# Kernel tuning notes

Hardware: AMD Instinct MI355X
Metric: run time of the kernel (lower is better)

## Reference

```python
import jax, jax.numpy as jnp
import numpy as np

B, S, D, H, L, FF, V, NB, G, C = 8, 1024, 256, 8, 2, 1024, 32000, 20000, 12, 4
DH = D // H


def _layer_norm(x, g, b, eps=1e-5):
    m = x.mean(-1, keepdims=True)
    v = ((x - m) ** 2).mean(-1, keepdims=True)
    return (x - m) / jnp.sqrt(v + eps) * g + b


def setup_inputs() -> dict:
    key = jax.random.key(0)
    ks = jax.random.split(key, 32)
    w = lambda k, shape, s=0.05: (jax.random.normal(k, shape, dtype=jnp.float32) * s)
    inp = {
        'input_ids': jax.random.randint(ks[0], (B, S), 0, V),
        'ngram_ids': jax.random.randint(ks[1], (V, G), 0, NB),
        'tfidf_scores': jax.random.uniform(ks[2], (V,), dtype=jnp.float32),
        'emb': jax.random.uniform(ks[3], (V, D), minval=-0.1, maxval=0.1, dtype=jnp.float32).at[0].set(0.0),  # padding_idx=0 row zeroed
        'pos_enc': jax.random.normal(ks[4], (1, S, D), dtype=jnp.float32) * 0.01,
        'bucket_emb': jax.random.uniform(ks[5], (NB, D), minval=-0.05, maxval=0.05, dtype=jnp.float32),
        'Wq': w(ks[6], (L, D, D)), 'bq': jnp.zeros((L, D)),
        'Wk': w(ks[7], (L, D, D)), 'bk': jnp.zeros((L, D)),
        'Wv': w(ks[8], (L, D, D)), 'bv': jnp.zeros((L, D)),
        'Wo': w(ks[9], (L, D, D)), 'bo': jnp.zeros((L, D)),
        'g1': jnp.ones((L, D)), 'be1': jnp.zeros((L, D)),
        'g2': jnp.ones((L, D)), 'be2': jnp.zeros((L, D)),
        'W1': w(ks[10], (L, D, FF)), 'b1': jnp.zeros((L, FF)),
        'W2': w(ks[11], (L, FF, D)), 'b2': jnp.zeros((L, D)),
        'alpha': jnp.full((L,), 0.1, dtype=jnp.float32),
        'gf': jnp.ones((D,)), 'bf': jnp.zeros((D,)),
        'Wc': jax.random.uniform(ks[12], (D, C), minval=-0.1, maxval=0.1, dtype=jnp.float32),
        'bc': jnp.zeros((C,)),
    }
    return inp


def reference(input_ids, ngram_ids, tfidf_scores, emb, pos_enc, bucket_emb,
              Wq, bq, Wk, bk, Wv, bv, Wo, bo, g1, be1, g2, be2,
              W1, b1, W2, b2, alpha, gf, bf, Wc, bc):
    pad_mask = input_ids == 0                      # (B,S) key padding mask
    x = emb[input_ids] + pos_enc[:, :S]            # (B,S,D)
    # char n-gram embedding: masked mean over n-gram buckets
    tok_ng = ngram_ids[jnp.clip(input_ids, 0, ngram_ids.shape[0] - 1)]   # (B,S,G)
    e_ng = bucket_emb[tok_ng]                       # (B,S,G,D)
    m = (tok_ng != 0)[..., None].astype(x.dtype)
    x = x + (e_ng * m).sum(axis=2) / jnp.clip(m.sum(axis=2), 1.0, None)
    # TF-IDF bias per key position
    bias_base = tfidf_scores[jnp.clip(input_ids, 0, tfidf_scores.shape[0] - 1)]  # (B,S)
    scale = DH ** -0.5
    for l in range(L):
        x2 = _layer_norm(x, g1[l], be1[l])
        Q = (x2 @ Wq[l] + bq[l]).reshape(B, S, H, DH).transpose(0, 2, 1, 3)
        K = (x2 @ Wk[l] + bk[l]).reshape(B, S, H, DH).transpose(0, 2, 1, 3)
        Vv = (x2 @ Wv[l] + bv[l]).reshape(B, S, H, DH).transpose(0, 2, 1, 3)
        scores = jnp.einsum('bhqd,bhkd->bhqk', Q, K) * scale
        scores = scores + (bias_base * alpha[l])[:, None, None, :]
        scores = jnp.where(pad_mask[:, None, None, :], -jnp.inf, scores)
        attn = jax.nn.softmax(scores, axis=-1)
        out = jnp.einsum('bhqk,bhkd->bhqd', attn, Vv).transpose(0, 2, 1, 3).reshape(B, S, D)
        x = x + (out @ Wo[l] + bo[l])
        x2 = _layer_norm(x, g2[l], be2[l])
        x = x + (jax.nn.relu(x2 @ W1[l] + b1[l]) @ W2[l] + b2[l])
    x = _layer_norm(x, gf, bf)
    return x[:, 0] @ Wc + bc                        # CLS pooling -> (B,4)
```

## Files before the change

### kernel.cpp

```cpp
#include <hip/hip_runtime.h>
#include <hip/hip_bf16.h>
#include <math.h>

#define TOK 8192
#define DIM 256
#define SEQ 1024
#define NH 8
#define FFD 1024
#define NL 2
#define VOCAB 32000
#define QKSTRIDE 2097152

typedef short bf16x8 __attribute__((ext_vector_type(8)));
typedef float f32x4 __attribute__((ext_vector_type(4)));

__device__ __forceinline__ ushort f2bf(float f) {
  union { float f; uint32_t u; } v; v.f = f;
  uint32_t r = v.u + 0x7FFFu + ((v.u >> 16) & 1u);
  return (ushort)(r >> 16);
}

__device__ __forceinline__ float bf2f(ushort u) {
  union { uint32_t u; float f; } v; v.u = (uint32_t)u << 16; return v.f;
}

__device__ __forceinline__ float exp2_n(float x) {
  float r; asm("v_exp_f32 %0, %1" : "=v"(r) : "v"(x)); return r;
}

__device__ __forceinline__ uint32_t cvtpk(float lo, float hi) {
  uint32_t r; asm("v_cvt_pk_bf16_f32 %0, %1, %2" : "=v"(r) : "v"(lo), "v"(hi));
  return r;
}

__device__ __forceinline__ void gload_lds16(const ushort* gp, ushort* lp) {
  __builtin_amdgcn_global_load_lds(
      (const __attribute__((address_space(1))) void*)gp,
      (__attribute__((address_space(3))) void*)lp, 16, 0, 0);
}

__global__ __launch_bounds__(256) void embed_ln_kernel(
    const int* __restrict__ ids, const int* __restrict__ ngram_ids,
    const float* __restrict__ tfidf, const float* __restrict__ emb,
    const float* __restrict__ pos, const float* __restrict__ bucket,
    const float* __restrict__ alpha, const float* __restrict__ g1,
    const float* __restrict__ be1,
    float* __restrict__ x, ushort* __restrict__ x2b, float* __restrict__ bm2)
{
  __shared__ int ngs[12];
  __shared__ float red[2][4];
  const int t = blockIdx.x;
  const int id = ids[t];
  int idc = id; if (idc < 0) idc = 0; if (idc > VOCAB-1) idc = VOCAB-1;
  if (threadIdx.x < 12) ngs[threadIdx.x] = ngram_ids[idc*12 + threadIdx.x];
  if (threadIdx.x == 0) {
    const float tf = tfidf[idc];
    const bool msk = (id == 0);
    const float l2e = 1.4426950408889634f;
    bm2[t]       = msk ? -1e30f : tf * alpha[0] * l2e;
    bm2[TOK + t] = msk ? -1e30f : tf * alpha[1] * l2e;
  }
  __syncthreads();
  const int d = threadIdx.x;
  const int s = t & (SEQ - 1);
  float v = emb[(size_t)id*DIM + d] + pos[s*DIM + d];
  float sum = 0.f; int cnt = 0;
  #pragma unroll
  for (int g = 0; g < 12; ++g) {
    const int ng = ngs[g];
    if (ng != 0) { sum += bucket[(size_t)ng*DIM + d]; cnt++; }
  }
  v += sum / fmaxf((float)cnt, 1.0f);
  x[(size_t)t*DIM + d] = v;
  const int wave = d >> 6, lane = d & 63;
  float sm = v;
  #pragma unroll
  for (int o = 32; o >= 1; o >>= 1) sm += __shfl_xor(sm, o);
  if (lane == 0) red[0][wave] = sm;
  __syncthreads();
  const float mean = (red[0][0]+red[0][1]+red[0][2]+red[0][3]) * (1.f/256.f);
  const float dv = v - mean;
  float q = dv * dv;
  #pragma unroll
  for (int o = 32; o >= 1; o >>= 1) q += __shfl_xor(q, o);
  if (lane == 0) red[1][wave] = q;
  __syncthreads();
  const float var = (red[1][0]+red[1][1]+red[1][2]+red[1][3]) * (1.f/256.f);
  const float rs = rsqrtf(var + 1e-5f);
  x2b[(size_t)t*DIM + d] = f2bf(dv*rs*g1[d] + be1[d]);
}

__global__ __launch_bounds__(256) void ln_bf16(
    const float* __restrict__ x, const float* __restrict__ g,
    const float* __restrict__ b, ushort* __restrict__ y)
{
  const int wave = threadIdx.x >> 6, lane = threadIdx.x & 63;
  const int row = blockIdx.x * 4 + wave;
  const float* xr = x + (size_t)row * DIM;
  float4 v = *reinterpret_cast<const float4*>(xr + lane*4);
  float s = v.x + v.y + v.z + v.w;
  #pragma unroll
  for (int o = 32; o >= 1; o >>= 1) s += __shfl_xor(s, o);
  const float mean = s * (1.f/256.f);
  const float dx0 = v.x-mean, dx1 = v.y-mean, dx2 = v.z-mean, dx3 = v.w-mean;
  float q = dx0*dx0 + dx1*dx1 + dx2*dx2 + dx3*dx3;
  #pragma unroll
  for (int o = 32; o >= 1; o >>= 1) q += __shfl_xor(q, o);
  const float rs = rsqrtf(q * (1.f/256.f) + 1e-5f);
  float4 gv = *reinterpret_cast<const float4*>(g + lane*4);
  float4 bv = *reinterpret_cast<const float4*>(b + lane*4);
  ushort4 o4;
  o4.x = f2bf(dx0*rs*gv.x + bv.x);
  o4.y = f2bf(dx1*rs*gv.y + bv.y);
  o4.z = f2bf(dx2*rs*gv.z + bv.z);
  o4.w = f2bf(dx3*rs*gv.w + bv.w);
  *reinterpret_cast<ushort4*>(y + (size_t)row*DIM + lane*4) = o4;
}

struct TDesc { const float* src; ushort* dst; int K; int N; };
struct TDescs { TDesc d[12]; };

__global__ __launch_bounds__(256) void transpose_conv(TDescs descs)
{
  const TDesc t = descs.d[blockIdx.z];
  const int k0 = blockIdx.x * 32, n0 = blockIdx.y * 32;
  if (k0 >= t.K || n0 >= t.N) return;
  __shared__ float tile[32][33];
  const int r = threadIdx.x >> 5, cc = threadIdx.x & 31;
  #pragma unroll
  for (int i = 0; i < 4; ++i)
    tile[r + i*8][cc] = t.src[(size_t)(k0 + r + i*8)*t.N + n0 + cc];
  __syncthreads();
  #pragma unroll
  for (int i = 0; i < 4; ++i)
    t.dst[(size_t)(n0 + r + i*8)*t.K + k0 + cc] = f2bf(tile[cc][r + i*8]);
}

template<int KDIM, int NDIM, int MODE>
__global__ __launch_bounds__(256) void gemm_mfma(
    const ushort* __restrict__ A, const ushort* __restrict__ Bw,
    const float* __restrict__ bias0, const float* __restrict__ bias1,
    const float* __restrict__ bias2, void* __restrict__ Cout,
    ushort* __restrict__ vtb)
{
  __shared__ ushort Al[3][64*32];
  __shared__ ushort Bl[3][128*32];
  const int bm = blockIdx.y * 64, bn = blockIdx.x * 128;
  const int tid = threadIdx.x, w = tid >> 6, lane = tid & 63;
  const int g = lane >> 4, c = lane & 15;
  const int lrow = lane >> 2, lc8 = (lane & 3) << 3;
  const f32x4 fzero = {0.f, 0.f, 0.f, 0.f};
  f32x4 acc[4][2];
  #pragma unroll
  for (int m = 0; m < 4; ++m) { acc[m][0] = fzero; acc[m][1] = fzero; }

#define STAGE(buf, k0)                                                         \
  {                                                                            \
    _Pragma("unroll")                                                          \
    for (int ch = w; ch < 12; ch += 4) {                                       \
      if (ch < 4)                                                              \
        gload_lds16(A + (size_t)(bm + ch*16 + lrow)*KDIM + (k0) + lc8,         \
                    &Al[buf][ch*512]);                                         \
      else                                                                     \
        gload_lds16(Bw + (size_t)(bn + (ch-4)*16 + lrow)*KDIM + (k0) + lc8,    \
                    &Bl[buf][(ch-4)*512]);                                     \
    }                                                                          \
  }

#define COMPUTE(buf)                                                           \
  {                                                                            \
    bf16x8 af[4], bfr[2];                                                      \
    _Pragma("unroll")                                                          \
    for (int m = 0; m < 4; ++m)                                                \
      af[m] = *(const bf16x8*)&Al[buf][(m*16 + c)*32 + g*8];                   \
    _Pragma("unroll")                                                          \
    for (int n = 0; n < 2; ++n)                                                \
      bfr[n] = *(const bf16x8*)&Bl[buf][(w*32 + n*16 + c)*32 + g*8];           \
    _Pragma("unroll")                                                          \
    for (int m = 0; m < 4; ++m)                                                \
      _Pragma("unroll")                                                        \
      for (int n = 0; n < 2; ++n)                                              \
        acc[m][n] = __builtin_amdgcn_mfma_f32_16x16x32_bf16(af[m], bfr[n], acc[m][n], 0, 0, 0); \
  }

  STAGE(0, 0);
  STAGE(1, 32);
  STAGE(2, 64);
  int buf = 0;
  for (int k0 = 0; k0 + 64 < KDIM; k0 += 32) {
    asm volatile("s_waitcnt vmcnt(6)" ::: "memory");
    __builtin_amdgcn_s_barrier();
    COMPUTE(buf);
    asm volatile("s_waitcnt lgkmcnt(0)" ::: "memory");
    __builtin_amdgcn_s_barrier();
    if (k0 + 96 < KDIM) STAGE(buf, k0 + 96);
    buf = (buf == 2) ? 0 : buf + 1;
  }
  asm volatile("s_waitcnt vmcnt(3)" ::: "memory");
  __builtin_amdgcn_s_barrier();
  COMPUTE(buf);
  buf = (buf == 2) ? 0 : buf + 1;
  asm volatile("s_waitcnt vmcnt(0)" ::: "memory");
  __builtin_amdgcn_s_barrier();
  COMPUTE(buf);
#undef STAGE
#undef COMPUTE

  #pragma unroll
  for (int m = 0; m < 4; ++m) {
    const int row0 = bm + m*16 + g*4;
    #pragma unroll
    for (int n = 0; n < 2; ++n) {
      const int col = bn + w*32 + n*16 + c;
      if (MODE == 1) {
        const float bb = bias0[col];
        #pragma unroll
        for (int r = 0; r < 4; ++r) {
          const float vv = fmaxf(acc[m][n][r] + bb, 0.f);
          const float other = __shfl_xor(vv, 1);
          if ((c & 1) == 0) {
            const uint32_t word = (uint32_t)f2bf(vv) | ((uint32_t)f2bf(other) << 16);
            *(uint32_t*)((ushort*)Cout + (size_t)(row0 + r)*NDIM + col) = word;
          }
        }
      } else if (MODE == 4) {
        const int b_ = row0 >> 10, s = row0 & (SEQ - 1);
        const int hd = col & 255;
        const int hh = hd >> 5, d = hd & 31;
        const float bb = (col < 256) ? bias0[hd] : bias1[hd];
        ushort* dst = ((col < 256) ? (ushort*)Cout : vtb)
                    + (((size_t)(b_*NH + hh)*SEQ + s) << 5) + d;
        #pragma unroll
        for (int r = 0; r < 4; ++r) {
          const float vv = acc[m][n][r] + bb;
          const float other = __shfl_xor(vv, 1);
          if ((c & 1) == 0) {
            const uint32_t word = (uint32_t)f2bf(vv) | ((uint32_t)f2bf(other) << 16);
            *(uint32_t*)(dst + (r << 5)) = word;
          }
        }
      } else {
        const int b_ = row0 >> 10, s = row0 & (SEQ - 1);
        if (col < 512) {
          const int hd = col & 255;
          const int hh = hd >> 5, d = hd & 31;
          const float bb = (col < 256) ? bias0[hd] : bias1[hd];
          ushort* dst = (ushort*)Cout + (col < 256 ? 0 : QKSTRIDE)
                      + (((size_t)(b_*NH + hh)*SEQ + s) << 5) + d;
          #pragma unroll
          for (int r = 0; r < 4; ++r) {
            const float vv = acc[m][n][r] + bb;
            const float other = __shfl_xor(vv, 1);
            if ((c & 1) == 0) {
              const uint32_t word = (uint32_t)f2bf(vv) | ((uint32_t)f2bf(other) << 16);
              *(uint32_t*)(dst + (r << 5)) = word;
            }
          }
        } else {
          const int hd = col - 512;
          const int hh = hd >> 5, d = hd & 31;
          const float bb = bias2[hd];
          const int sg = s >> 5, a = (s & 31) >> 2;
          const int pbase = (a & 3)*8 + (a >> 2)*4;
          ushort4 w4;
          w4.x = f2bf(acc[m][n][0] + bb);
          w4.y = f2bf(acc[m][n][1] + bb);
          w4.z = f2bf(acc[m][n][2] + bb);
          w4.w = f2bf(acc[m][n][3] + bb);
          *(ushort4*)(vtb + (((size_t)((b_*NH + hh)*32 + sg)*32 + d) << 5) + pbase) = w4;
        }
      }
    }
  }
}

template<int KDIM>
__global__ __launch_bounds__(256) void gemm64_acc(
    const ushort* __restrict__ A, const ushort* __restrict__ Bw,
    const float* __restrict__ bias, float* __restrict__ C)
{
  __shared__ ushort Al[3][64*32];
  __shared__ ushort Bl[3][64*32];
  const int bm = blockIdx.y * 64, bn = blockIdx.x * 64;
  const int tid = threadIdx.x, w = tid >> 6, lane = tid & 63;
  const int wm = w >> 1, wn = w & 1;
  const int g = lane >> 4, c = lane & 15;
  const int lrow = tid >> 2, lc8 = (tid & 3) << 3;
  const f32x4 fzero = {0.f, 0.f, 0.f, 0.f};
  f32x4 acc[2][2];
  acc[0][0] = fzero; acc[0][1] = fzero; acc[1][0] = fzero; acc[1][1] = fzero;

#define STAGE64(buf, k0)                                                       \
  {                                                                            \
    gload_lds16(A  + (size_t)(bm + lrow)*KDIM + (k0) + lc8,                    \
                &Al[buf][lrow*32 + lc8]);                                      \
    gload_lds16(Bw + (size_t)(bn + lrow)*KDIM + (k0) + lc8,                    \
                &Bl[buf][lrow*32 + lc8]);                                      \
  }

#define COMPUTE64(buf)                                                         \
  {                                                                            \
    bf16x8 af[2], bfr[2];                                                      \
    _Pragma("unroll")                                                          \
    for (int m = 0; m < 2; ++m)                                                \
      af[m] = *(const bf16x8*)&Al[buf][(wm*32 + m*16 + c)*32 + g*8];           \
    _Pragma("unroll")                                                          \
    for (int n = 0; n < 2; ++n)                                                \
      bfr[n] = *(const bf16x8*)&Bl[buf][(wn*32 + n*16 + c)*32 + g*8];          \
    _Pragma("unroll")                                                          \
    for (int m = 0; m < 2; ++m)                                                \
      _Pragma("unroll")                                                        \
      for (int n = 0; n < 2; ++n)                                              \
        acc[m][n] = __builtin_amdgcn_mfma_f32_16x16x32_bf16(af[m], bfr[n], acc[m][n], 0, 0, 0); \
  }

  STAGE64(0, 0);
  STAGE64(1, 32);
  STAGE64(2, 64);
  int buf = 0;
  for (int k0 = 0; k0 + 64 < KDIM; k0 += 32) {
    asm volatile("s_waitcnt vmcnt(4)" ::: "memory");
    __builtin_amdgcn_s_barrier();
    COMPUTE64(buf);
    asm volatile("s_waitcnt lgkmcnt(0)" ::: "memory");
    __builtin_amdgcn_s_barrier();
    if (k0 + 96 < KDIM) STAGE64(buf, k0 + 96);
    buf = (buf == 2) ? 0 : buf + 1;
  }
  asm volatile("s_waitcnt vmcnt(2)" ::: "memory");
  __builtin_amdgcn_s_barrier();
  COMPUTE64(buf);
  buf = (buf == 2) ? 0 : buf + 1;
  asm volatile("s_waitcnt vmcnt(0)" ::: "memory");
  __builtin_amdgcn_s_barrier();
  COMPUTE64(buf);
#undef STAGE64
#undef COMPUTE64

  #pragma unroll
  for (int m = 0; m < 2; ++m) {
    const int row0 = bm + wm*32 + m*16 + g*4;
    #pragma unroll
    for (int n = 0; n < 2; ++n) {
      const int col = bn + wn*32 + n*16 + c;
      const float bb = bias[col];
      #pragma unroll
      for (int r = 0; r < 4; ++r)
        C[(size_t)(row0 + r)*DIM + col] += acc[m][n][r] + bb;
    }
  }
}

__global__ __launch_bounds__(256) void attn_mfma(
    const ushort* __restrict__ qh, const ushort* __restrict__ kh,
    const ushort* __restrict__ vph, const float* __restrict__ bm2l,
    ushort* __restrict__ O)
{
  const int bid = blockIdx.x;
  const int lin = ((bid & 7) << 8) + (bid >> 3);
  const int tid = threadIdx.x, w = tid >> 6, lane = tid & 63;
  const int qw = lin & 31, h = (lin >> 5) & 7, b = lin >> 8;
  const int qb = qw << 5;
  const float scale2 = 0.17677669529663687f * 1.4426950408889634f;
  const int g = lane >> 4, c = lane & 15;
  const f32x4 fzero = {0.f, 0.f, 0.f, 0.f};
  const size_t bh = (size_t)(b*NH + h);

  const bf16x8 qf0 = *(const bf16x8*)(qh + ((bh*SEQ + qb + c)      << 5) + g*8);
  const bf16x8 qf1 = *(const bf16x8*)(qh + ((bh*SEQ + qb + 16 + c) << 5) + g*8);
  const ushort* kbase = kh  + ((bh*SEQ) << 5) + g*8;
  const ushort* vbase = vph + ((bh*SEQ) << 5) + g*8;
  const float*  bmb   = bm2l + b*SEQ;

  f32x4 oacc[2][2];
  oacc[0][0] = fzero; oacc[0][1] = fzero; oacc[1][0] = fzero; oacc[1][1] = fzero;
  float l0 = 0.f, l1 = 0.f;

  bf16x8 kfA[4], kfB[4];
  bf16x8 vfA[2][2], vfB[2][2];
  f32x4 bbA[4], bbB[4];

#define LOADT(kt, kf, vf, bb)                                                  \
  {                                                                            \
    _Pragma("unroll")                                                          \
    for (int ks = 0; ks < 4; ++ks) {                                           \
      kf[ks] = *(const bf16x8*)(kbase + (((kt) + ks*16 + c) << 5));            \
      bb[ks] = *(const f32x4*)(bmb + (kt) + ks*16 + g*4);                      \
    }                                                                          \
    _Pragma("unroll")                                                          \
    for (int ds_ = 0; ds_ < 2; ++ds_)                                          \
      _Pragma("unroll")                                                        \
      for (int sg = 0; sg < 2; ++sg)                                           \
        vf[ds_][sg] = *(const bf16x8*)(vbase +                                 \
            (((((kt) >> 5) + sg)*32 + ds_*16 + c) << 5));                      \
  }

#define ATILE(kf, vf, bb)                                                      \
  {                                                                            \
    f32x4 sf0[4], sf1[4];                                                      \
    __builtin_amdgcn_s_setprio(1);                                             \
    _Pragma("unroll")                                                          \
    for (int ks = 0; ks < 4; ++ks)                                             \
      sf0[ks] = __builtin_amdgcn_mfma_f32_16x16x32_bf16(kf[ks], qf0, fzero, 0, 0, 0); \
    _Pragma("unroll")                                                          \
    for (int ks = 0; ks < 4; ++ks)                                             \
      sf1[ks] = __builtin_amdgcn_mfma_f32_16x16x32_bf16(kf[ks], qf1, fzero, 0, 0, 0); \
    __builtin_amdgcn_s_setprio(0);                                             \
    float e0[4][4], e1[4][4];                                                  \
    _Pragma("unroll")                                                          \
    for (int ks = 0; ks < 4; ++ks)                                             \
      _Pragma("unroll")                                                        \
      for (int r = 0; r < 4; ++r) {                                            \
        e0[ks][r] = exp2_n(fmaf(sf0[ks][r], scale2, bb[ks][r]));               \
        e1[ks][r] = exp2_n(fmaf(sf1[ks][r], scale2, bb[ks][r]));               \
      }                                                                        \
    float a0 = 0.f, a1 = 0.f, a2 = 0.f, a3 = 0.f;                              \
    _Pragma("unroll")                                                          \
    for (int r = 0; r < 4; ++r) {                                              \
      a0 += e0[0][r] + e0[1][r]; a1 += e0[2][r] + e0[3][r];                    \
      a2 += e1[0][r] + e1[1][r]; a3 += e1[2][r] + e1[3][r];                    \
    }                                                                          \
    l0 += a0 + a1; l1 += a2 + a3;                                              \
    union { bf16x8 v; uint32_t u[4]; } p00, p01, p10, p11;                     \
    p00.u[0] = cvtpk(e0[0][0], e0[0][1]); p00.u[1] = cvtpk(e0[0][2], e0[0][3]);\
    p00.u[2] = cvtpk(e0[1][0], e0[1][1]); p00.u[3] = cvtpk(e0[1][2], e0[1][3]);\
    p01.u[0] = cvtpk(e0[2][0], e0[2][1]); p01.u[1] = cvtpk(e0[2][2], e0[2][3]);\
    p01.u[2] = cvtpk(e0[3][0], e0[3][1]); p01.u[3] = cvtpk(e0[3][2], e0[3][3]);\
    p10.u[0] = cvtpk(e1[0][0], e1[0][1]); p10.u[1] = cvtpk(e1[0][2], e1[0][3]);\
    p10.u[2] = cvtpk(e1[1][0], e1[1][1]); p10.u[3] = cvtpk(e1[1][2], e1[1][3]);\
    p11.u[0] = cvtpk(e1[2][0], e1[2][1]); p11.u[1] = cvtpk(e1[2][2], e1[2][3]);\
    p11.u[2] = cvtpk(e1[3][0], e1[3][1]); p11.u[3] = cvtpk(e1[3][2], e1[3][3]);\
    __builtin_amdgcn_s_setprio(1);                                             \
    oacc[0][0] = __builtin_amdgcn_mfma_f32_16x16x32_bf16(vf[0][0], p00.v, oacc[0][0], 0, 0, 0); \
    oacc[0][1] = __builtin_amdgcn_mfma_f32_16x16x32_bf16(vf[1][0], p00.v, oacc[0][1], 0, 0, 0); \
    oacc[1][0] = __builtin_amdgcn_mfma_f32_16x16x32_bf16(vf[0][0], p10.v, oacc[1][0], 0, 0, 0); \
    oacc[1][1] = __builtin_amdgcn_mfma_f32_16x16x32_bf16(vf[1][0], p10.v, oacc[1][1], 0, 0, 0); \
    oacc[0][0] = __builtin_amdgcn_mfma_f32_16x16x32_bf16(vf[0][1], p01.v, oacc[0][0], 0, 0, 0); \
    oacc[0][1] = __builtin_amdgcn_mfma_f32_16x16x32_bf16(vf[1][1], p01.v, oacc[0][1], 0, 0, 0); \
    oacc[1][0] = __builtin_amdgcn_mfma_f32_16x16x32_bf16(vf[0][1], p11.v, oacc[1][0], 0, 0, 0); \
    oacc[1][1] = __builtin_amdgcn_mfma_f32_16x16x32_bf16(vf[1][1], p11.v, oacc[1][1], 0, 0, 0); \
    __builtin_amdgcn_s_setprio(0);                                             \
  }

  const int kt0 = w << 8;
  LOADT(kt0, kfA, vfA, bbA);
  LOADT(kt0 + 64, kfB, vfB, bbB);
  ATILE(kfA, vfA, bbA);
  LOADT(kt0 + 128, kfA, vfA, bbA);
  ATILE(kfB, vfB, bbB);
  LOADT(kt0 + 192, kfB, vfB, bbB);
  ATILE(kfA, vfA, bbA);
  ATILE(kfB, vfB, bbB);
#undef LOADT
#undef ATILE

  __shared__ float Lo[4][64][19];
  #pragma unroll
  for (int q = 0; q < 2; ++q)
    #pragma unroll
    for (int ds_ = 0; ds_ < 2; ++ds_)
      #pragma unroll
      for (int i = 0; i < 4; ++i)
        Lo[w][lane][q*8 + ds_*4 + i] = oacc[q][ds_][i];
  Lo[w][lane][16] = l0;
  Lo[w][lane][17] = l1;
  __syncthreads();
  if (w < 2) {
    const int q = w;
    float o[8] = {0.f,0.f,0.f,0.f,0.f,0.f,0.f,0.f};
    float ls = 0.f;
    #pragma unroll
    for (int ww = 0; ww < 4; ++ww) {
      ls += Lo[ww][lane][16 + q];
      #pragma unroll
      for (int i = 0; i < 8; ++i) o[i] += Lo[ww][lane][q*8 + i];
    }
    ls += __shfl_xor(ls, 16);
    ls += __shfl_xor(ls, 32);
    const float inv = 1.f / ls;
    ushort* orow = O + (size_t)(b*SEQ + qb + q*16 + c)*DIM + h*32 + g*4;
    const uint32_t w0 = (uint32_t)f2bf(o[0]*inv) | ((uint32_t)f2bf(o[1]*inv) << 16);
    const uint32_t w1 = (uint32_t)f2bf(o[2]*inv) | ((uint32_t)f2bf(o[3]*inv) << 16);
    const uint32_t w2 = (uint32_t)f2bf(o[4]*inv) | ((uint32_t)f2bf(o[5]*inv) << 16);
    const uint32_t w3 = (uint32_t)f2bf(o[6]*inv) | ((uint32_t)f2bf(o[7]*inv) << 16);
    *(uint32_t*)(orow)      = w0;
    *(uint32_t*)(orow + 2)  = w1;
    *(uint32_t*)(orow + 16) = w2;
    *(uint32_t*)(orow + 18) = w3;
  }
}

__global__ __launch_bounds__(256) void decode512(
    const ushort* __restrict__ x2b, const ushort* __restrict__ Wq1,
    const float* __restrict__ bq1, const ushort* __restrict__ kh,
    const ushort* __restrict__ vh, const float* __restrict__ bm2l,
    float* __restrict__ P)
{
  const int lin = blockIdx.x;
  const int ks = lin & 3, bh = lin >> 2;
  const int b = bh >> 3, h = bh & 7;
  const int tid = threadIdx.x;
  const float scale2 = 0.17677669529663687f * 1.4426950408889634f;
  __shared__ float xrow[256];
  __shared__ float qv[32];
  xrow[tid] = bf2f(x2b[(size_t)(b*SEQ)*DIM + tid]);
  __syncthreads();
  if (tid < 32) {
    const ushort* wrow = Wq1 + (size_t)(h*32 + tid)*DIM;
    float acc = bq1[h*32 + tid];
    #pragma unroll
    for (int k8 = 0; k8 < 32; ++k8) {
      const bf16x8 wv = *(const bf16x8*)(wrow + k8*8);
      #pragma unroll
      for (int j = 0; j < 8; ++j)
        acc = fmaf(bf2f((ushort)wv[j]), xrow[k8*8 + j], acc);
    }
    qv[tid] = acc;
  }
  __syncthreads();
  const int key = ks*256 + tid;
  const ushort* kr = kh + (((size_t)bh*SEQ + key) << 5);
  float dot = 0.f;
  #pragma unroll
  for (int i = 0; i < 4; ++i) {
    const bf16x8 kv8 = *(const bf16x8*)(kr + i*8);
    #pragma unroll
    for (int j = 0; j < 8; ++j)
      dot = fmaf(bf2f((ushort)kv8[j]), qv[i*8 + j], dot);
  }
  const float e = exp2_n(fmaf(dot, scale2, bm2l[b*SEQ + key]));
  const ushort* vr = vh + (((size_t)bh*SEQ + key) << 5);
  __shared__ float red[256][33];
  #pragma unroll
  for (int i = 0; i < 4; ++i) {
    const bf16x8 vv8 = *(const bf16x8*)(vr + i*8);
    #pragma unroll
    for (int j = 0; j < 8; ++j)
      red[tid][i*8 + j] = e * bf2f((ushort)vv8[j]);
  }
  red[tid][32] = e;
  __syncthreads();
  for (int s = 128; s >= 1; s >>= 1) {
    for (int i = tid; i < s*33; i += 256) {
      const int r = i / 33, d = i - r*33;
      red[r][d] += red[r + s][d];
    }
    __syncthreads();
  }
  if (tid < 33) P[((size_t)bh*4 + ks)*33 + tid] = red[0][tid];
}

__global__ __launch_bounds__(256) void wo_part(
    const float* __restrict__ P, const ushort* __restrict__ WoT1,
    const float* __restrict__ bo1, float* __restrict__ wo_out)
{
  const int cc = blockIdx.x, tid = threadIdx.x;
  __shared__ float orow[8][256];
  {
    const int b = tid >> 5, d32 = tid & 31;
    #pragma unroll
    for (int h = 0; h < 8; ++h) {
      const float* pp = P + ((size_t)(b*8 + h)*4)*33;
      float ov = 0.f, l = 0.f;
      #pragma unroll
      for (int ks = 0; ks < 4; ++ks) { ov += pp[ks*33 + d32]; l += pp[ks*33 + 32]; }
      orow[b][h*32 + d32] = ov / l;
    }
  }
  __syncthreads();
  const int w = tid >> 6, lane = tid & 63;
  const int col = cc*4 + w;
  const ushort* wrow = WoT1 + (size_t)col*DIM + lane*4;
  float wk[4];
  #pragma unroll
  for (int j = 0; j < 4; ++j) wk[j] = bf2f(wrow[j]);
  #pragma unroll
  for (int b = 0; b < 8; ++b) {
    float p = 0.f;
    #pragma unroll
    for (int j = 0; j < 4; ++j) p = fmaf(wk[j], orow[b][lane*4 + j], p);
    #pragma unroll
    for (int off = 32; off >= 1; off >>= 1) p += __shfl_xor(p, off);
    if (lane == 0) wo_out[b*DIM + col] = p + bo1[col];
  }
}

__global__ __launch_bounds__(256) void ln2k(
    const float* __restrict__ x, const float* __restrict__ wo_out,
    const float* __restrict__ g21, const float* __restrict__ be21,
    float* __restrict__ newx_out, float* __restrict__ t2f)
{
  const int b = blockIdx.x, tid = threadIdx.x;
  const int wave = tid >> 6, lane = tid & 63;
  __shared__ float red[2][4];
  const float newx = x[(size_t)(b*SEQ)*DIM + tid] + wo_out[b*DIM + tid];
  newx_out[b*DIM + tid] = newx;
  float sm = newx;
  #pragma unroll
  for (int o = 32; o >= 1; o >>= 1) sm += __shfl_xor(sm, o);
  if (lane == 0) red[0][wave] = sm;
  __syncthreads();
  const float mean = (red[0][0]+red[0][1]+red[0][2]+red[0][3]) * (1.f/256.f);
  const float dv = newx - mean;
  float q = dv * dv;
  #pragma unroll
  for (int o = 32; o >= 1; o >>= 1) q += __shfl_xor(q, o);
  if (lane == 0) red[1][wave] = q;
  __syncthreads();
  const float var = (red[1][0]+red[1][1]+red[1][2]+red[1][3]) * (1.f/256.f);
  const float rs = rsqrtf(var + 1e-5f);
  t2f[b*DIM + tid] = dv*rs*g21[tid] + be21[tid];
}

__global__ __launch_bounds__(256) void ff1_part(
    const float* __restrict__ t2f, const ushort* __restrict__ W1T1,
    const float* __restrict__ b11, float* __restrict__ mid)
{
  const int cc = blockIdx.x, tid = threadIdx.x;
  __shared__ float trow[8][256];
  #pragma unroll
  for (int b = 0; b < 8; ++b) trow[b][tid] = t2f[b*DIM + tid];
  __syncthreads();
  const int dotid = tid >> 1;
  const int col = cc*16 + (dotid & 15);
  const int b = dotid >> 4;
  const int kh_ = (tid & 1) * 128;
  const ushort* wrow = W1T1 + (size_t)col*DIM + kh_;
  float acc = 0.f;
  #pragma unroll
  for (int k8 = 0; k8 < 16; ++k8) {
    const bf16x8 wv = *(const bf16x8*)(wrow + k8*8);
    #pragma unroll
    for (int j = 0; j < 8; ++j)
      acc = fmaf(bf2f((ushort)wv[j]), trow[b][kh_ + k8*8 + j], acc);
  }
  acc += __shfl_xor(acc, 1);
  if ((tid & 1) == 0) mid[b*FFD + col] = fmaxf(acc + b11[col], 0.f);
}

__global__ __launch_bounds__(256) void ff2_part(
    const float* __restrict__ mid, const ushort* __restrict__ W2T1,
    const float* __restrict__ b21, const float* __restrict__ newx_out,
    float* __restrict__ y2)
{
  const int cc = blockIdx.x, tid = threadIdx.x;
  __shared__ float mrow[8][1024];
  #pragma unroll
  for (int i = 0; i < 32; ++i) {
    const int idx = i*256 + tid;
    mrow[idx >> 10][idx & 1023] = mid[idx];
  }
  __syncthreads();
  const int dotid = tid >> 3;
  const int col = cc*4 + (dotid & 3);
  const int b = dotid >> 2;
  const int seg = (tid & 7) * 128;
  const ushort* wrow = W2T1 + (size_t)col*FFD + seg;
  float acc = 0.f;
  #pragma unroll
  for (int k8 = 0; k8 < 16; ++k8) {
    const bf16x8 wv = *(const bf16x8*)(wrow + k8*8);
    #pragma unroll
    for (int j = 0; j < 8; ++j)
      acc = fmaf(bf2f((ushort)wv[j]), mrow[b][seg + k8*8 + j], acc);
  }
  acc += __shfl_xor(acc, 1);
  acc += __shfl_xor(acc, 2);
  acc += __shfl_xor(acc, 4);
  if ((tid & 7) == 0)
    y2[b*DIM + col] = newx_out[b*DIM + col] + acc + b21[col];
}

__global__ __launch_bounds__(256) void cls2(
    const float* __restrict__ y2, const float* __restrict__ gf,
    const float* __restrict__ bfb, const float* __restrict__ Wc,
    const float* __restrict__ bc, float* __restrict__ out)
{
  const int b = blockIdx.x, tid = threadIdx.x;
  const int wave = tid >> 6, lane = tid & 63;
  const float v = y2[b*DIM + tid];
  __shared__ float redm[4], redv[4], redc[4][4];
  float s = v;
  #pragma unroll
  for (int o = 32; o >= 1; o >>= 1) s += __shfl_xor(s, o);
  if (lane == 0) redm[wave] = s;
  __syncthreads();
  const float mean = (redm[0]+redm[1]+redm[2]+redm[3]) * (1.f/256.f);
  const float dv = v - mean;
  float q = dv * dv;
  #pragma unroll
  for (int o = 32; o >= 1; o >>= 1) q += __shfl_xor(q, o);
  if (lane == 0) redv[wave] = q;
  __syncthreads();
  const float var = (redv[0]+redv[1]+redv[2]+redv[3]) * (1.f/256.f);
  const float rs = rsqrtf(var + 1e-5f);
  const float yn = dv*rs*gf[tid] + bfb[tid];
  float pc[4];
  #pragma unroll
  for (int cc = 0; cc < 4; ++cc) pc[cc] = yn * Wc[tid*4 + cc];
  #pragma unroll
  for (int cc = 0; cc < 4; ++cc) {
    #pragma unroll
    for (int o = 32; o >= 1; o >>= 1) pc[cc] += __shfl_xor(pc[cc], o);
  }
  if (lane == 0) {
    #pragma unroll
    for (int cc = 0; cc < 4; ++cc) redc[wave][cc] = pc[cc];
  }
  __syncthreads();
  if (tid < 4)
    out[b*4 + tid] = redc[0][tid] + redc[1][tid] + redc[2][tid] + redc[3][tid] + bc[tid];
}

extern "C" void kernel_launch(void* const* d_in, const int* in_sizes, int n_in,
                              void* d_out, int out_size, void* d_ws, size_t ws_size,
                              hipStream_t stream)
{
  const int*   ids    = (const int*)d_in[0];
  const int*   ngrams = (const int*)d_in[1];
  const float* tfidf  = (const float*)d_in[2];
  const float* emb    = (const float*)d_in[3];
  const float* pos    = (const float*)d_in[4];
  const float* bucket = (const float*)d_in[5];
  const float* Wq = (const float*)d_in[6];  const float* bq = (const float*)d_in[7];
  const float* Wk = (const float*)d_in[8];  const float* bk = (const float*)d_in[9];
  const float* Wv = (const float*)d_in[10]; const float* bv = (const float*)d_in[11];
  const float* Wo = (const float*)d_in[12]; const float* bo = (const float*)d_in[13];
  const float* g1 = (const float*)d_in[14]; const float* be1= (const float*)d_in[15];
  const float* g2 = (const float*)d_in[16]; const float* be2= (const float*)d_in[17];
  const float* W1 = (const float*)d_in[18]; const float* b1 = (const float*)d_in[19];
  const float* W2 = (const float*)d_in[20]; const float* b2 = (const float*)d_in[21];
  const float* alpha = (const float*)d_in[22];
  const float* gf = (const float*)d_in[23]; const float* bf = (const float*)d_in[24];
  const float* Wc = (const float*)d_in[25]; const float* bc = (const float*)d_in[26];

  uint8_t* base = (uint8_t*)d_ws;
  float*  x      = (float*)  base;
  ushort* x2b    = (ushort*)(base + 8388608);
  ushort* qkh    = (ushort*)(base + 12582912);
  ushort* vtb    = (ushort*)(base + 20971520);
  ushort* attb   = (ushort*)(base + 25165824);
  ushort* midb   = (ushort*)(base + 29360128);
  float*  bm2    = (float*) (base + 46137344);
  ushort* WqkvT  = (ushort*)(base + 46202880);
  ushort* WoT    = (ushort*)(base + 46989312);
  ushort* W1T    = (ushort*)(base + 47251456);
  ushort* W2T    = (ushort*)(base + 48300032);

  float* P       = (float*)(base + 25165824);
  float* wo_out  = (float*)(base + 25165824 + 65536);
  float* newxo   = (float*)(base + 25165824 + 73728);
  float* t2f     = (float*)(base + 25165824 + 81920);
  float* midf    = (float*)(base + 25165824 + 90112);
  float* y2      = (float*)(base + 25165824 + 122880);

  TDescs td;
  for (int l = 0; l < NL; ++l) {
    td.d[6*l+0] = { Wq + (size_t)l*DIM*DIM, WqkvT + (size_t)l*768*DIM +   0*DIM, DIM, DIM };
    td.d[6*l+1] = { Wk + (size_t)l*DIM*DIM, WqkvT + (size_t)l*768*DIM + 256*DIM, DIM, DIM };
    td.d[6*l+2] = { Wv + (size_t)l*DIM*DIM, WqkvT + (size_t)l*768*DIM + 512*DIM, DIM, DIM };
    td.d[6*l+3] = { Wo + (size_t)l*DIM*DIM, WoT  + (size_t)l*DIM*DIM,  DIM, DIM };
    td.d[6*l+4] = { W1 + (size_t)l*DIM*FFD, W1T  + (size_t)l*FFD*DIM,  DIM, FFD };
    td.d[6*l+5] = { W2 + (size_t)l*FFD*DIM, W2T  + (size_t)l*DIM*FFD,  FFD, DIM };
  }
  transpose_conv<<<dim3(32, 32, 12), 256, 0, stream>>>(td);

  embed_ln_kernel<<<TOK, 256, 0, stream>>>(
      ids, ngrams, tfidf, emb, pos, bucket, alpha, g1, be1, x, x2b, bm2);

  const dim3 gqkv(6, TOK/64), gkv(4, TOK/64), gff1(8, TOK/64), g64(4, TOK/64);

  gemm_mfma<256, 768, 3><<<gqkv, 256, 0, stream>>>(
      x2b, WqkvT, bq, bk, bv, qkh, vtb);
  attn_mfma<<<2048, 256, 0, stream>>>(qkh, qkh + QKSTRIDE, vtb, bm2, attb);
  gemm64_acc<256><<<g64, 256, 0, stream>>>(attb, WoT, bo, x);
  ln_bf16<<<TOK/4, 256, 0, stream>>>(x, g2, be2, x2b);
  gemm_mfma<256, 1024, 1><<<gff1, 256, 0, stream>>>(
      x2b, W1T, b1, nullptr, nullptr, midb, nullptr);
  gemm64_acc<1024><<<g64, 256, 0, stream>>>(midb, W2T, b2, x);

  ln_bf16<<<TOK/4, 256, 0, stream>>>(x, g1 + DIM, be1 + DIM, x2b);
  gemm_mfma<256, 512, 4><<<gkv, 256, 0, stream>>>(
      x2b, WqkvT + (size_t)768*DIM + 256*DIM, bk + DIM, bv + DIM, nullptr,
      qkh + QKSTRIDE, vtb);
  decode512<<<256, 256, 0, stream>>>(
      x2b, WqkvT + (size_t)768*DIM, bq + DIM,
      qkh + QKSTRIDE, vtb, bm2 + TOK, P);
  wo_part<<<64, 256, 0, stream>>>(P, WoT + DIM*DIM, bo + DIM, wo_out);
  ln2k<<<8, 256, 0, stream>>>(x, wo_out, g2 + DIM, be2 + DIM, newxo, t2f);
  ff1_part<<<64, 256, 0, stream>>>(t2f, W1T + FFD*DIM, b1 + FFD, midf);
  ff2_part<<<64, 256, 0, stream>>>(midf, W2T + DIM*FFD, b2 + DIM, newxo, y2);
  cls2<<<8, 256, 0, stream>>>(y2, gf, bf, Wc, bc, (float*)d_out);
}
```

Baseline: 150.4 us.

## Vectorize embed LN per-wave, defer attention bias loads, fuse ln2k into ff1

The embedding+LayerNorm kernel now handles one token per wave with float4 loads and shuffle-only reductions, which cuts block count and removes LDS barriers. The attention kernel stops prefetching the bias tiles into registers and loads them just before the exp step, lowering register pressure at the cost of exposed load latency. The small ln2k kernel is folded into ff1_part: each of the 64 blocks recomputes the residual and LayerNorm for the 8 CLS rows, and ff2_part recomputes the residual itself. This saves a launch and an intermediate buffer in exchange for redundant work.

```diff
diff --git a/kernel.cpp b/kernel.cpp
--- a/kernel.cpp
+++ b/kernel.cpp
@@ -47,13 +47,13 @@
     const float* __restrict__ be1,
     float* __restrict__ x, ushort* __restrict__ x2b, float* __restrict__ bm2)
 {
-  __shared__ int ngs[12];
-  __shared__ float red[2][4];
-  const int t = blockIdx.x;
+  __shared__ int ngs[4][12];
+  const int wave = threadIdx.x >> 6, lane = threadIdx.x & 63;
+  const int t = blockIdx.x * 4 + wave;
   const int id = ids[t];
   int idc = id; if (idc < 0) idc = 0; if (idc > VOCAB-1) idc = VOCAB-1;
-  if (threadIdx.x < 12) ngs[threadIdx.x] = ngram_ids[idc*12 + threadIdx.x];
-  if (threadIdx.x == 0) {
+  if (lane < 12) ngs[wave][lane] = ngram_ids[idc*12 + lane];
+  if (lane == 0) {
     const float tf = tfidf[idc];
     const bool msk = (id == 0);
     const float l2e = 1.4426950408889634f;
@@ -61,33 +61,41 @@
     bm2[TOK + t] = msk ? -1e30f : tf * alpha[1] * l2e;
   }
   __syncthreads();
-  const int d = threadIdx.x;
+  const int d0 = lane * 4;
   const int s = t & (SEQ - 1);
-  float v = emb[(size_t)id*DIM + d] + pos[s*DIM + d];
-  float sum = 0.f; int cnt = 0;
+  float4 v = *reinterpret_cast<const float4*>(emb + (size_t)id*DIM + d0);
+  const float4 p4 = *reinterpret_cast<const float4*>(pos + s*DIM + d0);
+  v.x += p4.x; v.y += p4.y; v.z += p4.z; v.w += p4.w;
+  float4 sum = {0.f, 0.f, 0.f, 0.f}; int cnt = 0;
   #pragma unroll
   for (int g = 0; g < 12; ++g) {
-    const int ng = ngs[g];
-    if (ng != 0) { sum += bucket[(size_t)ng*DIM + d]; cnt++; }
-  }
-  v += sum / fmaxf((float)cnt, 1.0f);
-  x[(size_t)t*DIM + d] = v;
-  const int wave = d >> 6, lane = d & 63;
-  float sm = v;
+    const int ng = ngs[wave][g];
+    if (ng != 0) {
+      const float4 b4 = *reinterpret_cast<const float4*>(bucket + (size_t)ng*DIM + d0);
+      sum.x += b4.x; sum.y += b4.y; sum.z += b4.z; sum.w += b4.w;
+      cnt++;
+    }
+  }
+  const float inv = 1.f / fmaxf((float)cnt, 1.0f);
+  v.x += sum.x*inv; v.y += sum.y*inv; v.z += sum.z*inv; v.w += sum.w*inv;
+  *reinterpret_cast<float4*>(x + (size_t)t*DIM + d0) = v;
+  float sm = v.x + v.y + v.z + v.w;
   #pragma unroll
   for (int o = 32; o >= 1; o >>= 1) sm += __shfl_xor(sm, o);
-  if (lane == 0) red[0][wave] = sm;
-  __syncthreads();
-  const float mean = (red[0][0]+red[0][1]+red[0][2]+red[0][3]) * (1.f/256.f);
-  const float dv = v - mean;
-  float q = dv * dv;
+  const float mean = sm * (1.f/256.f);
+  const float dx0 = v.x-mean, dx1 = v.y-mean, dx2 = v.z-mean, dx3 = v.w-mean;
+  float q = dx0*dx0 + dx1*dx1 + dx2*dx2 + dx3*dx3;
   #pragma unroll
   for (int o = 32; o >= 1; o >>= 1) q += __shfl_xor(q, o);
-  if (lane == 0) red[1][wave] = q;
-  __syncthreads();
-  const float var = (red[1][0]+red[1][1]+red[1][2]+red[1][3]) * (1.f/256.f);
-  const float rs = rsqrtf(var + 1e-5f);
-  x2b[(size_t)t*DIM + d] = f2bf(dv*rs*g1[d] + be1[d]);
+  const float rs = rsqrtf(q * (1.f/256.f) + 1e-5f);
+  const float4 gv = *reinterpret_cast<const float4*>(g1 + d0);
+  const float4 bv = *reinterpret_cast<const float4*>(be1 + d0);
+  ushort4 o4;
+  o4.x = f2bf(dx0*rs*gv.x + bv.x);
+  o4.y = f2bf(dx1*rs*gv.y + bv.y);
+  o4.z = f2bf(dx2*rs*gv.z + bv.z);
+  o4.w = f2bf(dx3*rs*gv.w + bv.w);
+  *reinterpret_cast<ushort4*>(x2b + (size_t)t*DIM + d0) = o4;
 }
 
 __global__ __launch_bounds__(256) void ln_bf16(
@@ -378,15 +386,12 @@
 
   bf16x8 kfA[4], kfB[4];
   bf16x8 vfA[2][2], vfB[2][2];
-  f32x4 bbA[4], bbB[4];
-
-#define LOADT(kt, kf, vf, bb)                                                  \
+
+#define LOADT(kt, kf, vf)                                                      \
   {                                                                            \
     _Pragma("unroll")                                                          \
-    for (int ks = 0; ks < 4; ++ks) {                                           \
+    for (int ks = 0; ks < 4; ++ks)                                             \
       kf[ks] = *(const bf16x8*)(kbase + (((kt) + ks*16 + c) << 5));            \
-      bb[ks] = *(const f32x4*)(bmb + (kt) + ks*16 + g*4);                      \
-    }                                                                          \
     _Pragma("unroll")                                                          \
     for (int ds_ = 0; ds_ < 2; ++ds_)                                          \
       _Pragma("unroll")                                                        \
@@ -395,7 +400,7 @@
             (((((kt) >> 5) + sg)*32 + ds_*16 + c) << 5));                      \
   }
 
-#define ATILE(kf, vf, bb)                                                      \
+#define ATILE(kf, vf, kt)                                                      \
   {                                                                            \
     f32x4 sf0[4], sf1[4];                                                      \
     __builtin_amdgcn_s_setprio(1);                                             \
@@ -408,12 +413,14 @@
     __builtin_amdgcn_s_setprio(0);                                             \
     float e0[4][4], e1[4][4];                                                  \
     _Pragma("unroll")                                                          \
-    for (int ks = 0; ks < 4; ++ks)                                             \
+    for (int ks = 0; ks < 4; ++ks) {                                           \
+      const f32x4 bb = *(const f32x4*)(bmb + (kt) + ks*16 + g*4);              \
       _Pragma("unroll")                                                        \
       for (int r = 0; r < 4; ++r) {                                            \
-        e0[ks][r] = exp2_n(fmaf(sf0[ks][r], scale2, bb[ks][r]));               \
-        e1[ks][r] = exp2_n(fmaf(sf1[ks][r], scale2, bb[ks][r]));               \
+        e0[ks][r] = exp2_n(fmaf(sf0[ks][r], scale2, bb[r]));                   \
+        e1[ks][r] = exp2_n(fmaf(sf1[ks][r], scale2, bb[r]));                   \
       }                                                                        \
+    }                                                                          \
     float a0 = 0.f, a1 = 0.f, a2 = 0.f, a3 = 0.f;                              \
     _Pragma("unroll")                                                          \
     for (int r = 0; r < 4; ++r) {                                              \
@@ -443,14 +450,14 @@
   }
 
   const int kt0 = w << 8;
-  LOADT(kt0, kfA, vfA, bbA);
-  LOADT(kt0 + 64, kfB, vfB, bbB);
-  ATILE(kfA, vfA, bbA);
-  LOADT(kt0 + 128, kfA, vfA, bbA);
-  ATILE(kfB, vfB, bbB);
-  LOADT(kt0 + 192, kfB, vfB, bbB);
-  ATILE(kfA, vfA, bbA);
-  ATILE(kfB, vfB, bbB);
+  LOADT(kt0, kfA, vfA);
+  LOADT(kt0 + 64, kfB, vfB);
+  ATILE(kfA, vfA, kt0);
+  LOADT(kt0 + 128, kfA, vfA);
+  ATILE(kfB, vfB, kt0 + 64);
+  LOADT(kt0 + 192, kfB, vfB);
+  ATILE(kfA, vfA, kt0 + 128);
+  ATILE(kfB, vfB, kt0 + 192);
 #undef LOADT
 #undef ATILE
 
@@ -585,41 +592,41 @@
   }
 }
 
-__global__ __launch_bounds__(256) void ln2k(
+__global__ __launch_bounds__(256) void ff1_part(
     const float* __restrict__ x, const float* __restrict__ wo_out,
     const float* __restrict__ g21, const float* __restrict__ be21,
-    float* __restrict__ newx_out, float* __restrict__ t2f)
-{
-  const int b = blockIdx.x, tid = threadIdx.x;
+    const ushort* __restrict__ W1T1, const float* __restrict__ b11,
+    float* __restrict__ mid)
+{
+  const int cc = blockIdx.x, tid = threadIdx.x;
   const int wave = tid >> 6, lane = tid & 63;
-  __shared__ float red[2][4];
-  const float newx = x[(size_t)(b*SEQ)*DIM + tid] + wo_out[b*DIM + tid];
-  newx_out[b*DIM + tid] = newx;
-  float sm = newx;
-  #pragma unroll
-  for (int o = 32; o >= 1; o >>= 1) sm += __shfl_xor(sm, o);
-  if (lane == 0) red[0][wave] = sm;
-  __syncthreads();
-  const float mean = (red[0][0]+red[0][1]+red[0][2]+red[0][3]) * (1.f/256.f);
-  const float dv = newx - mean;
-  float q = dv * dv;
-  #pragma unroll
-  for (int o = 32; o >= 1; o >>= 1) q += __shfl_xor(q, o);
-  if (lane == 0) red[1][wave] = q;
-  __syncthreads();
-  const float var = (red[1][0]+red[1][1]+red[1][2]+red[1][3]) * (1.f/256.f);
-  const float rs = rsqrtf(var + 1e-5f);
-  t2f[b*DIM + tid] = dv*rs*g21[tid] + be21[tid];
-}
-
-__global__ __launch_bounds__(256) void ff1_part(
-    const float* __restrict__ t2f, const ushort* __restrict__ W1T1,
-    const float* __restrict__ b11, float* __restrict__ mid)
-{
-  const int cc = blockIdx.x, tid = threadIdx.x;
   __shared__ float trow[8][256];
   #pragma unroll
-  for (int b = 0; b < 8; ++b) trow[b][tid] = t2f[b*DIM + tid];
+  for (int b = 0; b < 8; ++b)
+    trow[b][tid] = x[(size_t)(b*SEQ)*DIM + tid] + wo_out[b*DIM + tid];
+  __syncthreads();
+  #pragma unroll
+  for (int bb_ = 0; bb_ < 2; ++bb_) {
+    const int b = wave + bb_*4;
+    float4 vv = *(float4*)&trow[b][lane*4];
+    float sm = vv.x + vv.y + vv.z + vv.w;
+    #pragma unroll
+    for (int o = 32; o >= 1; o >>= 1) sm += __shfl_xor(sm, o);
+    const float mean = sm * (1.f/256.f);
+    const float dx0 = vv.x-mean, dx1 = vv.y-mean, dx2 = vv.z-mean, dx3 = vv.w-mean;
+    float q = dx0*dx0 + dx1*dx1 + dx2*dx2 + dx3*dx3;
+    #pragma unroll
+    for (int o = 32; o >= 1; o >>= 1) q += __shfl_xor(q, o);
+    const float rs = rsqrtf(q * (1.f/256.f) + 1e-5f);
+    const float4 gv = *(const float4*)(g21 + lane*4);
+    const float4 bv = *(const float4*)(be21 + lane*4);
+    float4 nv;
+    nv.x = dx0*rs*gv.x + bv.x;
+    nv.y = dx1*rs*gv.y + bv.y;
+    nv.z = dx2*rs*gv.z + bv.z;
+    nv.w = dx3*rs*gv.w + bv.w;
+    *(float4*)&trow[b][lane*4] = nv;
+  }
   __syncthreads();
   const int dotid = tid >> 1;
   const int col = cc*16 + (dotid & 15);
@@ -640,8 +647,8 @@
 
 __global__ __launch_bounds__(256) void ff2_part(
     const float* __restrict__ mid, const ushort* __restrict__ W2T1,
-    const float* __restrict__ b21, const float* __restrict__ newx_out,
-    float* __restrict__ y2)
+    const float* __restrict__ b21, const float* __restrict__ x,
+    const float* __restrict__ wo_out, float* __restrict__ y2)
 {
   const int cc = blockIdx.x, tid = threadIdx.x;
   __shared__ float mrow[8][1024];
@@ -668,7 +675,8 @@
   acc += __shfl_xor(acc, 2);
   acc += __shfl_xor(acc, 4);
   if ((tid & 7) == 0)
-    y2[b*DIM + col] = newx_out[b*DIM + col] + acc + b21[col];
+    y2[b*DIM + col] = x[(size_t)(b*SEQ)*DIM + col] + wo_out[b*DIM + col]
+                    + acc + b21[col];
 }
 
 __global__ __launch_bounds__(256) void cls2(
@@ -749,8 +757,6 @@
 
   float* P       = (float*)(base + 25165824);
   float* wo_out  = (float*)(base + 25165824 + 65536);
-  float* newxo   = (float*)(base + 25165824 + 73728);
-  float* t2f     = (float*)(base + 25165824 + 81920);
   float* midf    = (float*)(base + 25165824 + 90112);
   float* y2      = (float*)(base + 25165824 + 122880);
 
@@ -765,7 +771,7 @@
   }
   transpose_conv<<<dim3(32, 32, 12), 256, 0, stream>>>(td);
 
-  embed_ln_kernel<<<TOK, 256, 0, stream>>>(
+  embed_ln_kernel<<<TOK/4, 256, 0, stream>>>(
       ids, ngrams, tfidf, emb, pos, bucket, alpha, g1, be1, x, x2b, bm2);
 
   const dim3 gqkv(6, TOK/64), gkv(4, TOK/64), gff1(8, TOK/64), g64(4, TOK/64);
@@ -787,8 +793,8 @@
       x2b, WqkvT + (size_t)768*DIM, bq + DIM,
       qkh + QKSTRIDE, vtb, bm2 + TOK, P);
   wo_part<<<64, 256, 0, stream>>>(P, WoT + DIM*DIM, bo + DIM, wo_out);
-  ln2k<<<8, 256, 0, stream>>>(x, wo_out, g2 + DIM, be2 + DIM, newxo, t2f);
-  ff1_part<<<64, 256, 0, stream>>>(t2f, W1T + FFD*DIM, b1 + FFD, midf);
-  ff2_part<<<64, 256, 0, stream>>>(midf, W2T + DIM*FFD, b2 + DIM, newxo, y2);
+  ff1_part<<<64, 256, 0, stream>>>(x, wo_out, g2 + DIM, be2 + DIM,
+                                   W1T + FFD*DIM, b1 + FFD, midf);
+  ff2_part<<<64, 256, 0, stream>>>(midf, W2T + DIM*FFD, b2 + DIM, x, wo_out, y2);
   cls2<<<8, 256, 0, stream>>>(y2, gf, bf, Wc, bc, (float*)d_out);
 }
```

Result: faster. 143.7 us (-4.5%).
